# Performance work log

Measured on AMD Instinct MI355X. Metric: run time of the kernel, lower is better.

## Reference

```python
import jax, jax.numpy as jnp
import numpy as np

B, N, C = 4, 4096, 1024
H, HC = 16, 64
R = int(HC * np.log(HC))  # 266 random features
EPS = 1e-3


def _orthogonal_projection(num_rows, num_cols, seed=0):
    # Block-orthogonal random matrix: QR of gaussian blocks, rows concatenated.
    rng = np.random.default_rng(seed)
    blocks = []
    n_full = num_rows // num_cols
    for _ in range(n_full):
        q, _ = np.linalg.qr(rng.standard_normal((num_cols, num_cols)))
        blocks.append(q.T)
    remain = num_rows - n_full * num_cols
    if remain > 0:
        q, _ = np.linalg.qr(rng.standard_normal((num_cols, num_cols)))
        blocks.append(q.T[:remain])
    return np.concatenate(blocks, axis=0).astype(np.float32)  # (num_rows, num_cols)


def setup_inputs() -> dict:
    key = jax.random.key(0)
    ks = jax.random.split(key, 6)
    scale = 0.02
    return {
        "x": jax.random.normal(ks[0], (B, N, C), dtype=jnp.float32),
        "Wq": jax.random.normal(ks[1], (C, H * HC), dtype=jnp.float32) * scale,
        "Wk": jax.random.normal(ks[2], (C, H * HC), dtype=jnp.float32) * scale,
        "Wv": jax.random.normal(ks[3], (C, H * HC), dtype=jnp.float32) * scale,
        "Wo": jax.random.normal(ks[4], (H * HC, C), dtype=jnp.float32) * scale,
        "bo": jnp.zeros((C,), dtype=jnp.float32),
        "proj": jnp.asarray(_orthogonal_projection(R, HC, seed=0)),
    }


def reference(x, Wq, Wk, Wv, Wo, bo, proj):
    b, n, _ = x.shape
    # qkv projections, split heads: (B, H, N, HC)
    q = (x @ Wq).reshape(b, n, H, HC).transpose(0, 2, 1, 3)
    k = (x @ Wk).reshape(b, n, H, HC).transpose(0, 2, 1, 3)
    v = (x @ Wv).reshape(b, n, H, HC).transpose(0, 2, 1, 3)
    # FAVOR+ generalized kernel: relu(x @ proj^T) + eps -> (B, H, N, R)
    qp = jax.nn.relu(jnp.einsum('bhnd,rd->bhnr', q, proj)) + EPS
    kp = jax.nn.relu(jnp.einsum('bhnd,rd->bhnr', k, proj)) + EPS
    # linear attention: O(N) in sequence length
    k_sum = kp.sum(axis=-2)                                   # (B, H, R)
    d_inv = 1.0 / jnp.einsum('bhnr,bhr->bhn', qp, k_sum)      # (B, H, N)
    kv = jnp.einsum('bhnr,bhnd->bhrd', kp, v)                 # (B, H, R, HC)
    qkv = jnp.einsum('bhnr,bhrd->bhnd', qp, kv)               # (B, H, N, HC)
    out = qkv * d_inv[..., None]
    # merge heads and output projection
    out = out.transpose(0, 2, 1, 3).reshape(b, n, H * HC)
    return out @ Wo + bo
```

## Files before the change

kernel.cpp:

```cpp
#include <hip/hip_runtime.h>
#include <hip/hip_bf16.h>


typedef __bf16 bf16x8 __attribute__((ext_vector_type(8)));
typedef unsigned short u16x8 __attribute__((ext_vector_type(8)));
typedef float  f32x4  __attribute__((ext_vector_type(4)));

#define EPS_F 1e-3f

__device__ __forceinline__ void gld16(const void* g, void* l) {
  __builtin_amdgcn_global_load_lds(
      (const __attribute__((address_space(1))) void*)g,
      (__attribute__((address_space(3))) void*)l, 16, 0, 0);
}

template <int EPI>
__global__ void __launch_bounds__(512, 2)
gemm256(const __hip_bfloat16* __restrict__ A, long lda,
        const __hip_bfloat16* __restrict__ Bt, long ldb,
        void* __restrict__ Cp, long ldc,
        int Mtiles, int Ntiles, int K, const float* __restrict__ bias) {
  __shared__ __align__(16) char sm[131072];

  const int tid  = threadIdx.x;
  const int lane = tid & 63;
  const int wave = tid >> 6;
  const int wm   = wave >> 2;
  const int wn   = wave & 3;
  const int quad = lane >> 4;
  const int l15  = lane & 15;

  const int bid = blockIdx.x;
  const int Mx  = Mtiles >> 3;
  const int xcd = bid & 7;
  const int wl  = bid >> 3;
  const int gsz = Mx << 2;
  const int grp = wl / gsz;
  const int rr  = wl - grp * gsz;
  const int mt  = xcd * Mx + (rr % Mx);
  const int nt  = (grp << 2) + (rr / Mx);
  const long m0 = (long)mt * 256;
  const long n0 = (long)nt * 256;

  const int srow = tid >> 3;
  const int sg   = (tid & 7) ^ (srow & 7);
  const __hip_bfloat16* aS = A  + (m0 + srow) * lda + sg * 8;
  const __hip_bfloat16* bS = Bt + (n0 + srow) * ldb + sg * 8;
  char* smc = (char*)sm;
  const int ldsOff = tid * 16;

  const int aRowB = (wm * 128 + l15) * 128;
  const int bRowB = 32768 + (wn * 64 + l15) * 128;
  const int sw    = (l15 & 7) << 4;
  const int cx0   = (quad * 16) ^ sw;
  const int cx1   = (64 + quad * 16) ^ sw;

  f32x4 acc[8][4] = {};

#define GLD_A(pp, kk, i)                                                   \
  gld16(aS + (long)(i) * 64 * lda + (kk),                                  \
        smc + (pp) * 65536 + (i) * 8192 + ldsOff);
#define GLD_B(pp, kk, i)                                                   \
  gld16(bS + (long)(i) * 64 * ldb + (kk),                                  \
        smc + (pp) * 65536 + 32768 + (i) * 8192 + ldsOff);

#define QCL(AR, BR, accI, accJ)                                            \
  __builtin_amdgcn_s_setprio(1);                                           \
  _Pragma("unroll") for (int it = 0; it < 4; ++it)                         \
      _Pragma("unroll") for (int jt = 0; jt < 2; ++jt)                     \
          acc[(accI) + it][(accJ) + jt] =                                  \
              __builtin_amdgcn_mfma_f32_16x16x32_bf16(                     \
                  AR[it], BR[jt], acc[(accI) + it][(accJ) + jt], 0, 0, 0); \
  __builtin_amdgcn_s_setprio(0);

  const int NT = K >> 6;
#pragma unroll
  for (int i = 0; i < 4; ++i) { GLD_A(0, 0, i) GLD_B(0, 0, i) }
#pragma unroll
  for (int i = 0; i < 4; ++i) { GLD_A(1, 64, i) GLD_B(1, 64, i) }
  asm volatile("s_waitcnt vmcnt(8)" ::: "memory");
  __builtin_amdgcn_s_barrier();
  asm volatile("" ::: "memory");

  bf16x8 a0k0[4], a1k0[4], a0k1[4], a1k1[4];
  bf16x8 b01k0[2], b23k0[2], b01k1[2], b23k1[2];
#pragma unroll
  for (int jt = 0; jt < 2; ++jt)
    b01k0[jt] = *(const bf16x8*)(smc + bRowB + jt * 2048 + cx0);
#pragma unroll
  for (int it = 0; it < 4; ++it)
    a0k0[it] = *(const bf16x8*)(smc + aRowB + it * 2048 + cx0);

  int p = 0;
  for (int t = 0; t < NT; ++t) {
    const char* base  = smc + p * 65536;
    const char* nbase = smc + (p ^ 1) * 65536;
    const long kk = (long)(t + 2) * 64;
    const bool pf = (t + 2 < NT);

#pragma unroll
    for (int jt = 0; jt < 2; ++jt)
      b23k0[jt] = *(const bf16x8*)(base + bRowB + (jt + 2) * 2048 + cx0);
    QCL(a0k0, b01k0, 0, 0)
#pragma unroll
    for (int it = 0; it < 4; ++it)
      a1k0[it] = *(const bf16x8*)(base + aRowB + (4 + it) * 2048 + cx0);
    QCL(a0k0, b23k0, 0, 2)
#pragma unroll
    for (int jt = 0; jt < 2; ++jt)
      b01k1[jt] = *(const bf16x8*)(base + bRowB + jt * 2048 + cx1);
#pragma unroll
    for (int it = 0; it < 4; ++it)
      a0k1[it] = *(const bf16x8*)(base + aRowB + it * 2048 + cx1);
    QCL(a1k0, b01k0, 4, 0)
#pragma unroll
    for (int jt = 0; jt < 2; ++jt)
      b23k1[jt] = *(const bf16x8*)(base + bRowB + (jt + 2) * 2048 + cx1);
    QCL(a1k0, b23k0, 4, 2)
#pragma unroll
    for (int it = 0; it < 4; ++it)
      a1k1[it] = *(const bf16x8*)(base + aRowB + (4 + it) * 2048 + cx1);
    QCL(a0k1, b01k1, 0, 0)
    QCL(a0k1, b23k1, 0, 2)
    asm volatile("s_waitcnt lgkmcnt(0)" ::: "memory");
    __builtin_amdgcn_s_barrier();
    asm volatile("" ::: "memory");
    if (pf) {
      GLD_A(p, kk, 0) GLD_A(p, kk, 1) GLD_A(p, kk, 2) GLD_A(p, kk, 3)
      GLD_B(p, kk, 0) GLD_B(p, kk, 1) GLD_B(p, kk, 2) GLD_B(p, kk, 3)
    }
    QCL(a1k1, b01k1, 4, 0)
    if (pf) {
      asm volatile("s_waitcnt vmcnt(8)" ::: "memory");
    } else {
      asm volatile("s_waitcnt vmcnt(0)" ::: "memory");
    }
    __builtin_amdgcn_s_barrier();
    asm volatile("" ::: "memory");
    if (t + 1 < NT) {
#pragma unroll
      for (int jt = 0; jt < 2; ++jt)
        b01k0[jt] = *(const bf16x8*)(nbase + bRowB + jt * 2048 + cx0);
#pragma unroll
      for (int it = 0; it < 4; ++it)
        a0k0[it] = *(const bf16x8*)(nbase + aRowB + it * 2048 + cx0);
    }
    QCL(a1k1, b23k1, 4, 2)
    p ^= 1;
  }
#undef GLD_A
#undef GLD_B
#undef QCL

  if constexpr (EPI == 7) {
    __hip_bfloat16* Cb = (__hip_bfloat16*)Cp;
    const long slab  = (n0 >> 10) * 16777216;
    const long ncol0 = (n0 & 1023) + wn * 64 + l15;
#pragma unroll
    for (int it = 0; it < 8; ++it) {
#pragma unroll
      for (int i = 0; i < 4; ++i) {
        const long gm = m0 + wm * 128 + it * 16 + quad * 4 + i;
        __hip_bfloat16* rowp = Cb + slab + gm * 1024 + ncol0;
#pragma unroll
        for (int jt = 0; jt < 4; ++jt)
          rowp[jt * 16] = (__hip_bfloat16)acc[it][jt][i];
      }
    }
  } else if constexpr (EPI == 5) {
    float* Cf = (float*)Cp;
    float bv[4];
#pragma unroll
    for (int jt = 0; jt < 4; ++jt)
      bv[jt] = bias[n0 + wn * 64 + jt * 16 + l15];
#pragma unroll
    for (int it = 0; it < 8; ++it) {
#pragma unroll
      for (int i = 0; i < 4; ++i) {
        const long gm = m0 + wm * 128 + it * 16 + quad * 4 + i;
        float* rowp = Cf + gm * ldc + n0 + wn * 64 + l15;
#pragma unroll
        for (int jt = 0; jt < 4; ++jt)
          rowp[jt * 16] = acc[it][jt][i] + bv[jt];
      }
    }
  }
}

__global__ void __launch_bounds__(512, 2)
favor_kv(const __hip_bfloat16* __restrict__ Kb,
         const __hip_bfloat16* __restrict__ Vb,
         const __hip_bfloat16* __restrict__ projb_g,
         float* __restrict__ kvp) {
  __shared__ __align__(16) char sm[147456];
  char* Pj  = sm;
  char* KtB = sm + 36864;
  char* KPB = sm + 53248;
  char* VTB = sm + 126976;

  const int tid  = threadIdx.x;
  const int lane = tid & 63;
  const int wave = tid >> 6;
  const int quad = lane >> 4;
  const int l15  = lane & 15;
  const int swL  = (l15 & 7) << 4;

  const int bh   = blockIdx.x & 63;
  const int slab = blockIdx.x >> 6;
  const int b    = bh >> 4, h = bh & 15;
  const long rowbase = (long)b * 4096 + (long)slab * 1024;

  for (int p = 0; p < 5; ++p) {
    const int idx = p * 512 + tid;
    if (idx < 2304) {
      const int r = idx >> 3, g = (idx & 7) ^ (r & 7);
      gld16(projb_g + r * 64 + g * 8, Pj + idx * 16);
    }
  }
#pragma unroll
  for (int q = 0; q < 2; ++q) {
    unsigned short* vth = (unsigned short*)(VTB + q * 10240 + 64 * 128);
    for (int i = tid; i < 1024; i += 512) vth[i] = (i < 64) ? 0x3F80 : 0;
  }

  const int rK = tid >> 3, gK = (tid & 7) ^ (rK & 7);
  const int nl = tid >> 3, seg = tid & 7;
  gld16(Kb + (rowbase + rK) * 1024 + h * 64 + gK * 8, KtB + tid * 16);
  u16x8 vc = *(const u16x8*)(Vb + (rowbase + nl) * 1024 + h * 64 + seg * 8);

  const int wm1 = wave & 3;
  const int wn1 = wave >> 2;
  const int nJ  = (wave < 2) ? 3 : 2;

  f32x4 acc2[3][5] = {};

#define KV_GEMM2(KPo, VTo)                                                   \
  _Pragma("unroll") for (int ks = 0; ks < 2; ++ks) {                         \
    const int cb = ks * 64 + quad * 16;                                      \
    bf16x8 bfr2[5];                                                          \
    _Pragma("unroll") for (int fd = 0; fd < 5; ++fd) {                       \
      const int d = fd * 16 + l15;                                           \
      const int s2 = ((d & 7) ^ ((d >> 3) & 7)) << 4;                        \
      bfr2[fd] = *(const bf16x8*)((VTo) + d * 128 + (cb ^ s2));              \
    }                                                                        \
    _Pragma("unroll") for (int j = 0; j < 3; ++j) {                          \
      if (j < nJ) {                                                          \
        const int r2 = (wave + 8 * j) * 16 + l15;                            \
        const bf16x8 af2 =                                                   \
            *(const bf16x8*)((KPo) + r2 * 128 + (cb ^ ((r2 & 7) << 4)));     \
        _Pragma("unroll") for (int fd = 0; fd < 5; ++fd)                     \
            acc2[j][fd] = __builtin_amdgcn_mfma_f32_16x16x32_bf16(           \
                af2, bfr2[fd], acc2[j][fd], 0, 0, 0);                        \
      }                                                                      \
    }                                                                        \
  }

  for (int t = 0; t < 16; ++t) {
    const int q = t & 1;
    char* Kt  = KtB + q * 8192;
    char* KP  = KPB + q * 36864;
    char* VT  = VTB + q * 10240;
    char* KPo = KPB + (q ^ 1) * 36864;
    char* VTo = VTB + (q ^ 1) * 10240;

    asm volatile("s_waitcnt vmcnt(0)" ::: "memory");
    __builtin_amdgcn_s_barrier();
    asm volatile("" ::: "memory");

#pragma unroll
    for (int j = 0; j < 8; ++j) {
      const int d = seg * 8 + j;
      const int s = ((d & 7) ^ ((d >> 3) & 7)) << 4;
      *(unsigned short*)(VT + d * 128 + ((nl * 2) ^ s)) = vc[j];
    }
    if (t < 15) {
      const long nb1 = rowbase + (long)(t + 1) * 64;
      gld16(Kb + (nb1 + rK) * 1024 + h * 64 + gK * 8,
            KtB + (q ^ 1) * 8192 + tid * 16);
      vc = *(const u16x8*)(Vb + (nb1 + nl) * 1024 + h * 64 + seg * 8);
    }
    f32x4 acc1[9] = {};
#pragma unroll
    for (int ks = 0; ks < 2; ++ks) {
      const int cb = ks * 64 + quad * 16;
      const bf16x8 af1 =
          *(const bf16x8*)(Kt + (wm1 * 16 + l15) * 128 + (cb ^ swL));
      bf16x8 bfr[9];
#pragma unroll
      for (int fn = 0; fn < 9; ++fn)
        bfr[fn] = *(const bf16x8*)(Pj + (wn1 * 144 + fn * 16 + l15) * 128 +
                                   (cb ^ swL));
#pragma unroll
      for (int fn = 0; fn < 9; ++fn)
        acc1[fn] = __builtin_amdgcn_mfma_f32_16x16x32_bf16(af1, bfr[fn],
                                                           acc1[fn], 0, 0, 0);
    }
    {
      const int nb = (wm1 * 16 + quad * 4) * 2;
#pragma unroll
      for (int fn = 0; fn < 9; ++fn) {
        const int r = wn1 * 144 + fn * 16 + l15;
        const bool ok = (r < 266);
        union { __hip_bfloat16 hh[4]; uint2 u; } pk;
#pragma unroll
        for (int ii = 0; ii < 4; ++ii) {
          float v = acc1[fn][ii];
          v = ok ? (fmaxf(v, 0.f) + EPS_F) : 0.f;
          pk.hh[ii] = (__hip_bfloat16)v;
        }
        *(uint2*)(KP + r * 128 + (nb ^ ((r & 7) << 4))) = pk.u;
      }
    }
    if (t > 0) { KV_GEMM2(KPo, VTo) }
    asm volatile("s_waitcnt lgkmcnt(0)" ::: "memory");
    __builtin_amdgcn_s_barrier();
    asm volatile("" ::: "memory");
  }
  { KV_GEMM2(KPB + 36864, VTB + 10240) }
#undef KV_GEMM2

  float* dst = kvp + (long)blockIdx.x * 23040;
#pragma unroll
  for (int j = 0; j < 3; ++j) {
    if (j < nJ) {
      const int rb = (wave + 8 * j) * 16 + quad * 4;
#pragma unroll
      for (int fd = 0; fd < 5; ++fd) {
        const int d = fd * 16 + l15;
#pragma unroll
        for (int ii = 0; ii < 4; ++ii)
          dst[(long)(rb + ii) * 80 + d] = acc2[j][fd][ii];
      }
    }
  }
}

__global__ void __launch_bounds__(256)
finalize_kvx2(const float* __restrict__ kvp,
              __hip_bfloat16* __restrict__ kvxb) {
  __shared__ float lf[288 * 21];
  const int bh = blockIdx.x >> 2, dq = blockIdx.x & 3, t = threadIdx.x;
  for (int p = 0; p < 23; ++p) {
    const int q = p * 256 + t;
    if (q < 5760) {
      const int r = q / 20, dl = q - r * 20;
      float s = 0.f;
#pragma unroll
      for (int sl = 0; sl < 4; ++sl)
        s += kvp[(long)(sl * 64 + bh) * 23040 + r * 80 + dq * 20 + dl];
      lf[r * 21 + dl] = s;
    }
  }
  __syncthreads();
  for (int p = 0; p < 23; ++p) {
    const int o = p * 256 + t;
    if (o < 5760) {
      const int dl = o / 288, r = o - dl * 288;
      kvxb[(long)bh * 23040 + (long)(dq * 20 + dl) * 288 + r] =
          (__hip_bfloat16)lf[r * 21 + dl];
    }
  }
}

__global__ void __launch_bounds__(512, 2)
favor_out(const __hip_bfloat16* __restrict__ Qb,
          const __hip_bfloat16* __restrict__ kvxb_g,
          const __hip_bfloat16* __restrict__ projb_g,
          __hip_bfloat16* __restrict__ outm) {
  __shared__ __align__(16) char sm[160512];
  char* Pj = sm;
  char* KX = sm + 36864;
  char* QP = sm + 84224;
  float* Dsh = (float*)(sm + 160000);

  const int tid  = threadIdx.x;
  const int lane = tid & 63;
  const int wave = tid >> 6;
  const int quad = lane >> 4;
  const int l15  = lane & 15;
  const int swL  = (l15 & 7) << 4;

  const int bh  = blockIdx.x >> 3;
  const int rb8 = blockIdx.x & 7;
  const int b = bh >> 4, h = bh & 15;
  const long rowbase = (long)b * 4096 + (long)rb8 * 512;

  for (int p = 0; p < 5; ++p) {
    const int idx = p * 512 + tid;
    if (idx < 2304) {
      const int r = idx >> 3, g = (idx & 7) ^ (r & 7);
      gld16(projb_g + r * 64 + g * 8, Pj + idx * 16);
    }
  }
  {
    const __hip_bfloat16* src = kvxb_g + (long)bh * 23040;
#pragma unroll
    for (int p = 0; p < 6; ++p) {
      const int idx = p * 512 + tid;
      if (idx < 2880) {
        const int d = idx / 36, g = idx % 36;
        const bf16x8 v = *(const bf16x8*)(src + d * 288 + g * 8);
        *(bf16x8*)(KX + d * 592 + g * 16) = v;
      }
    }
  }
  const int rS = tid >> 3, gS = (tid & 7) ^ (rS & 7);
  const int rS2 = rS + 64, gS2 = (tid & 7) ^ (rS2 & 7);
  u16x8 qv0 = *(const u16x8*)(Qb + (rowbase + rS) * 1024 + h * 64 + gS * 8);
  u16x8 qv1 = *(const u16x8*)(Qb + (rowbase + rS2) * 1024 + h * 64 + gS2 * 8);

  const int wm1 = wave >> 2;
  const int wn1 = wave & 3;

  for (int s = 0; s < 4; ++s) {
    *(u16x8*)(QP + tid * 16) = qv0;
    *(u16x8*)(QP + 8192 + tid * 16) = qv1;
    asm volatile("s_waitcnt lgkmcnt(0)" ::: "memory");
    if (s == 0) asm volatile("s_waitcnt vmcnt(0)" ::: "memory");
    __builtin_amdgcn_s_barrier();
    asm volatile("" ::: "memory");
    f32x4 acc1[9][2] = {};
#pragma unroll
    for (int ks = 0; ks < 2; ++ks) {
      const int cb = ks * 64 + quad * 16;
      bf16x8 bfr[2];
#pragma unroll
      for (int fn = 0; fn < 2; ++fn)
        bfr[fn] = *(const bf16x8*)(QP + (wn1 * 32 + fn * 16 + l15) * 128 +
                                   (cb ^ swL));
      bf16x8 af[9];
#pragma unroll
      for (int fm = 0; fm < 9; ++fm)
        af[fm] = *(const bf16x8*)(Pj + (wm1 * 144 + fm * 16 + l15) * 128 +
                                  (cb ^ swL));
#pragma unroll
      for (int fm = 0; fm < 9; ++fm)
#pragma unroll
        for (int fn = 0; fn < 2; ++fn)
          acc1[fm][fn] = __builtin_amdgcn_mfma_f32_16x16x32_bf16(
              af[fm], bfr[fn], acc1[fm][fn], 0, 0, 0);
    }
    if (s < 3) {
      const long n1 = (long)(s + 1) * 128;
      qv0 = *(const u16x8*)(Qb + (rowbase + n1 + rS) * 1024 + h * 64 + gS * 8);
      qv1 = *(const u16x8*)(Qb + (rowbase + n1 + rS2) * 1024 + h * 64 +
                            gS2 * 8);
    }
    __builtin_amdgcn_s_barrier();
    asm volatile("" ::: "memory");
#pragma unroll
    for (int fm = 0; fm < 9; ++fm) {
      const int r0 = wm1 * 144 + fm * 16 + quad * 4;
#pragma unroll
      for (int fn = 0; fn < 2; ++fn) {
        const int n = wn1 * 32 + fn * 16 + l15;
        union { __hip_bfloat16 hh[4]; uint2 u; } pk;
#pragma unroll
        for (int ii = 0; ii < 4; ++ii) {
          float v = acc1[fm][fn][ii];
          v = (r0 + ii < 266) ? (fmaxf(v, 0.f) + EPS_F) : 0.f;
          pk.hh[ii] = (__hip_bfloat16)v;
        }
        *(uint2*)(QP + n * 592 + r0 * 2) = pk.u;
      }
    }
    asm volatile("s_waitcnt lgkmcnt(0)" ::: "memory");
    __builtin_amdgcn_s_barrier();
    asm volatile("" ::: "memory");
    f32x4 acc2[5] = {};
#pragma unroll
    for (int ks = 0; ks < 9; ++ks) {
      const int cb = ks * 64 + quad * 16;
      const bf16x8 af = *(const bf16x8*)(QP + (wave * 16 + l15) * 592 + cb);
      bf16x8 bfr[5];
#pragma unroll
      for (int fd = 0; fd < 5; ++fd)
        bfr[fd] = *(const bf16x8*)(KX + (fd * 16 + l15) * 592 + cb);
#pragma unroll
      for (int fd = 0; fd < 5; ++fd)
        acc2[fd] = __builtin_amdgcn_mfma_f32_16x16x32_bf16(af, bfr[fd],
                                                           acc2[fd], 0, 0, 0);
    }
    if (l15 == 0) {
#pragma unroll
      for (int ii = 0; ii < 4; ++ii)
        Dsh[wave * 16 + quad * 4 + ii] = acc2[4][ii];
    }
    asm volatile("s_waitcnt lgkmcnt(0)" ::: "memory");
    __builtin_amdgcn_s_barrier();
    asm volatile("" ::: "memory");
#pragma unroll
    for (int ii = 0; ii < 4; ++ii) {
      const int nloc = wave * 16 + quad * 4 + ii;
      const float den = Dsh[nloc];
      const float dinv = (den > 1e-30f) ? (1.f / den) : 0.f;
      __hip_bfloat16* rowp =
          outm + (rowbase + (long)s * 128 + nloc) * 1024 + h * 64;
#pragma unroll
      for (int fd = 0; fd < 4; ++fd)
        rowp[fd * 16 + l15] = (__hip_bfloat16)(acc2[fd][ii] * dinv);
    }
  }
}

__global__ void cvt_x(const float* __restrict__ x,
                      __hip_bfloat16* __restrict__ xb) {
  const long i = ((long)blockIdx.x * 256 + threadIdx.x) * 8;
  const float4 f0 = *(const float4*)(x + i);
  const float4 f1 = *(const float4*)(x + i + 4);
  union { __hip_bfloat16 h[8]; uint4 u; } r;
  r.h[0] = (__hip_bfloat16)f0.x; r.h[1] = (__hip_bfloat16)f0.y;
  r.h[2] = (__hip_bfloat16)f0.z; r.h[3] = (__hip_bfloat16)f0.w;
  r.h[4] = (__hip_bfloat16)f1.x; r.h[5] = (__hip_bfloat16)f1.y;
  r.h[6] = (__hip_bfloat16)f1.z; r.h[7] = (__hip_bfloat16)f1.w;
  *(uint4*)(xb + i) = r.u;
}

__global__ void prep_w(const float* __restrict__ s0,
                       const float* __restrict__ s1,
                       const float* __restrict__ s2,
                       const float* __restrict__ s3,
                       const float* __restrict__ proj,
                       __hip_bfloat16* __restrict__ dq,
                       __hip_bfloat16* __restrict__ dwo,
                       __hip_bfloat16* __restrict__ projb) {
  const int z = blockIdx.z;
  if (z == 4) {
    const int i = (blockIdx.y * 32 + blockIdx.x) * 256 + (int)threadIdx.x;
    if (i < 288 * 64) {
      const int r = i >> 6;
      __hip_bfloat16 v = (__hip_bfloat16)0.f;
      if (r < 266) v = (__hip_bfloat16)proj[i];
      projb[i] = v;
    }
    return;
  }
  __shared__ float t[32][33];
  const float* src = (z == 0) ? s0 : (z == 1) ? s1 : (z == 2) ? s2 : s3;
  __hip_bfloat16* dst = (z < 3) ? (dq + (long)z * 1048576) : dwo;
  const int k0 = blockIdx.x * 32, n0 = blockIdx.y * 32;
  const int tx = threadIdx.x & 31, ty = threadIdx.x >> 5;
#pragma unroll
  for (int i = 0; i < 4; ++i)
    t[ty + i * 8][tx] = src[(long)(k0 + ty + i * 8) * 1024 + n0 + tx];
  __syncthreads();
#pragma unroll
  for (int i = 0; i < 4; ++i)
    dst[(long)(n0 + ty + i * 8) * 1024 + k0 + tx] =
        (__hip_bfloat16)t[tx][ty + i * 8];
}

extern "C" void kernel_launch(void* const* d_in, const int* in_sizes, int n_in,
                              void* d_out, int out_size, void* d_ws,
                              size_t ws_size, hipStream_t stream) {
  const float* x    = (const float*)d_in[0];
  const float* Wq   = (const float*)d_in[1];
  const float* Wk   = (const float*)d_in[2];
  const float* Wv   = (const float*)d_in[3];
  const float* Wo   = (const float*)d_in[4];
  const float* bo   = (const float*)d_in[5];
  const float* proj = (const float*)d_in[6];
  float* out = (float*)d_out;
  char* ws = (char*)d_ws;

  constexpr long o_wqkvt = 0;
  constexpr long o_wot   = 6291456;
  constexpr long o_projb = 8388608;
  constexpr long o_Qb    = 8425472;
  constexpr long o_Kb    = 41979904;
  constexpr long o_Vb    = 75534336;
  constexpr long o_xb    = 109088768;
  constexpr long o_kvp   = 109088768;
  constexpr long o_kvxb  = 132681728;

  __hip_bfloat16* wqkvt = (__hip_bfloat16*)(ws + o_wqkvt);
  __hip_bfloat16* wot   = (__hip_bfloat16*)(ws + o_wot);
  __hip_bfloat16* projb = (__hip_bfloat16*)(ws + o_projb);
  __hip_bfloat16* Qb    = (__hip_bfloat16*)(ws + o_Qb);
  __hip_bfloat16* Kb    = (__hip_bfloat16*)(ws + o_Kb);
  __hip_bfloat16* Vb    = (__hip_bfloat16*)(ws + o_Vb);
  __hip_bfloat16* xb    = (__hip_bfloat16*)(ws + o_xb);
  float*          kvp   = (float*)(ws + o_kvp);
  __hip_bfloat16* kvxb  = (__hip_bfloat16*)(ws + o_kvxb);
  __hip_bfloat16* outm  = Kb;

  cvt_x<<<8192, 256, 0, stream>>>(x, xb);
  prep_w<<<dim3(32, 32, 5), 256, 0, stream>>>(Wq, Wk, Wv, Wo, proj, wqkvt,
                                              wot, projb);

  gemm256<7><<<768, 512, 0, stream>>>(xb, 1024, wqkvt, 1024, Qb, 0, 64, 12,
                                      1024, nullptr);

  favor_kv<<<256, 512, 0, stream>>>(Kb, Vb, projb, kvp);
  finalize_kvx2<<<256, 256, 0, stream>>>(kvp, kvxb);

  favor_out<<<512, 512, 0, stream>>>(Qb, kvxb, projb, outm);

  gemm256<5><<<256, 512, 0, stream>>>(outm, 1024, wot, 1024, out, 1024, 64, 4,
                                      1024, bo);
}
```

Baseline: 367.3 us.

## Double-buffer Q tiles via async LDS loads and read kv straight from global

```diff
diff --git a/kernel.cpp b/kernel.cpp
--- a/kernel.cpp
+++ b/kernel.cpp
@@ -367,11 +367,10 @@
           const __hip_bfloat16* __restrict__ kvxb_g,
           const __hip_bfloat16* __restrict__ projb_g,
           __hip_bfloat16* __restrict__ outm) {
-  __shared__ __align__(16) char sm[160512];
-  char* Pj = sm;
-  char* KX = sm + 36864;
-  char* QP = sm + 84224;
-  float* Dsh = (float*)(sm + 160000);
+  __shared__ __align__(16) char sm[145408];
+  char* Pj  = sm;
+  char* QbL = sm + 36864;
+  char* QP  = sm + 69632;
 
   const int tid  = threadIdx.x;
   const int lane = tid & 63;
@@ -384,6 +383,7 @@
   const int rb8 = blockIdx.x & 7;
   const int b = bh >> 4, h = bh & 15;
   const long rowbase = (long)b * 4096 + (long)rb8 * 512;
+  const __hip_bfloat16* kx = kvxb_g + (long)bh * 23040;
 
   for (int p = 0; p < 5; ++p) {
     const int idx = p * 512 + tid;
@@ -392,31 +392,18 @@
       gld16(projb_g + r * 64 + g * 8, Pj + idx * 16);
     }
   }
-  {
-    const __hip_bfloat16* src = kvxb_g + (long)bh * 23040;
-#pragma unroll
-    for (int p = 0; p < 6; ++p) {
-      const int idx = p * 512 + tid;
-      if (idx < 2880) {
-        const int d = idx / 36, g = idx % 36;
-        const bf16x8 v = *(const bf16x8*)(src + d * 288 + g * 8);
-        *(bf16x8*)(KX + d * 592 + g * 16) = v;
-      }
-    }
-  }
   const int rS = tid >> 3, gS = (tid & 7) ^ (rS & 7);
   const int rS2 = rS + 64, gS2 = (tid & 7) ^ (rS2 & 7);
-  u16x8 qv0 = *(const u16x8*)(Qb + (rowbase + rS) * 1024 + h * 64 + gS * 8);
-  u16x8 qv1 = *(const u16x8*)(Qb + (rowbase + rS2) * 1024 + h * 64 + gS2 * 8);
+  gld16(Qb + (rowbase + rS) * 1024 + h * 64 + gS * 8, QbL + tid * 16);
+  gld16(Qb + (rowbase + rS2) * 1024 + h * 64 + gS2 * 8, QbL + 8192 + tid * 16);
 
   const int wm1 = wave >> 2;
   const int wn1 = wave & 3;
 
   for (int s = 0; s < 4; ++s) {
-    *(u16x8*)(QP + tid * 16) = qv0;
-    *(u16x8*)(QP + 8192 + tid * 16) = qv1;
-    asm volatile("s_waitcnt lgkmcnt(0)" ::: "memory");
-    if (s == 0) asm volatile("s_waitcnt vmcnt(0)" ::: "memory");
+    const int q = s & 1;
+    const char* Qcur = QbL + q * 16384;
+    asm volatile("s_waitcnt vmcnt(0)" ::: "memory");
     __builtin_amdgcn_s_barrier();
     asm volatile("" ::: "memory");
     f32x4 acc1[9][2] = {};
@@ -426,7 +413,7 @@
       bf16x8 bfr[2];
 #pragma unroll
       for (int fn = 0; fn < 2; ++fn)
-        bfr[fn] = *(const bf16x8*)(QP + (wn1 * 32 + fn * 16 + l15) * 128 +
+        bfr[fn] = *(const bf16x8*)(Qcur + (wn1 * 32 + fn * 16 + l15) * 128 +
                                    (cb ^ swL));
       bf16x8 af[9];
 #pragma unroll
@@ -441,13 +428,12 @@
               af[fm], bfr[fn], acc1[fm][fn], 0, 0, 0);
     }
     if (s < 3) {
-      const long n1 = (long)(s + 1) * 128;
-      qv0 = *(const u16x8*)(Qb + (rowbase + n1 + rS) * 1024 + h * 64 + gS * 8);
-      qv1 = *(const u16x8*)(Qb + (rowbase + n1 + rS2) * 1024 + h * 64 +
-                            gS2 * 8);
-    }
-    __builtin_amdgcn_s_barrier();
-    asm volatile("" ::: "memory");
+      const long n1 = rowbase + (long)(s + 1) * 128;
+      gld16(Qb + (n1 + rS) * 1024 + h * 64 + gS * 8,
+            QbL + (q ^ 1) * 16384 + tid * 16);
+      gld16(Qb + (n1 + rS2) * 1024 + h * 64 + gS2 * 8,
+            QbL + (q ^ 1) * 16384 + 8192 + tid * 16);
+    }
 #pragma unroll
     for (int fm = 0; fm < 9; ++fm) {
       const int r0 = wm1 * 144 + fm * 16 + quad * 4;
@@ -475,25 +461,18 @@
       bf16x8 bfr[5];
 #pragma unroll
       for (int fd = 0; fd < 5; ++fd)
-        bfr[fd] = *(const bf16x8*)(KX + (fd * 16 + l15) * 592 + cb);
+        bfr[fd] = *(const bf16x8*)(kx + (fd * 16 + l15) * 288 + ks * 32 +
+                                   quad * 8);
 #pragma unroll
       for (int fd = 0; fd < 5; ++fd)
         acc2[fd] = __builtin_amdgcn_mfma_f32_16x16x32_bf16(af, bfr[fd],
                                                            acc2[fd], 0, 0, 0);
     }
-    if (l15 == 0) {
-#pragma unroll
-      for (int ii = 0; ii < 4; ++ii)
-        Dsh[wave * 16 + quad * 4 + ii] = acc2[4][ii];
-    }
-    asm volatile("s_waitcnt lgkmcnt(0)" ::: "memory");
-    __builtin_amdgcn_s_barrier();
-    asm volatile("" ::: "memory");
 #pragma unroll
     for (int ii = 0; ii < 4; ++ii) {
+      const float den = __shfl(acc2[4][ii], quad << 4, 64);
+      const float dinv = (den > 1e-30f) ? (1.f / den) : 0.f;
       const int nloc = wave * 16 + quad * 4 + ii;
-      const float den = Dsh[nloc];
-      const float dinv = (den > 1e-30f) ? (1.f / den) : 0.f;
       __hip_bfloat16* rowp =
           outm + (rowbase + (long)s * 128 + nloc) * 1024 + h * 64;
 #pragma unroll
```

Measured after the change: 395.4 us. 1.08x slower.

## Load Q fragments directly from global and broadcast denominators via shuffles

Applied to the files above, without the earlier changes.

```diff
diff --git a/kernel.cpp b/kernel.cpp
--- a/kernel.cpp
+++ b/kernel.cpp
@@ -362,16 +362,15 @@
   }
 }
 
-__global__ void __launch_bounds__(512, 2)
+__global__ void __launch_bounds__(512, 1)
 favor_out(const __hip_bfloat16* __restrict__ Qb,
           const __hip_bfloat16* __restrict__ kvxb_g,
           const __hip_bfloat16* __restrict__ projb_g,
           __hip_bfloat16* __restrict__ outm) {
-  __shared__ __align__(16) char sm[160512];
+  __shared__ __align__(16) char sm[160000];
   char* Pj = sm;
   char* KX = sm + 36864;
   char* QP = sm + 84224;
-  float* Dsh = (float*)(sm + 160000);
 
   const int tid  = threadIdx.x;
   const int lane = tid & 63;
@@ -404,21 +403,13 @@
       }
     }
   }
-  const int rS = tid >> 3, gS = (tid & 7) ^ (rS & 7);
-  const int rS2 = rS + 64, gS2 = (tid & 7) ^ (rS2 & 7);
-  u16x8 qv0 = *(const u16x8*)(Qb + (rowbase + rS) * 1024 + h * 64 + gS * 8);
-  u16x8 qv1 = *(const u16x8*)(Qb + (rowbase + rS2) * 1024 + h * 64 + gS2 * 8);
+  __syncthreads();
 
   const int wm1 = wave >> 2;
   const int wn1 = wave & 3;
 
   for (int s = 0; s < 4; ++s) {
-    *(u16x8*)(QP + tid * 16) = qv0;
-    *(u16x8*)(QP + 8192 + tid * 16) = qv1;
-    asm volatile("s_waitcnt lgkmcnt(0)" ::: "memory");
-    if (s == 0) asm volatile("s_waitcnt vmcnt(0)" ::: "memory");
-    __builtin_amdgcn_s_barrier();
-    asm volatile("" ::: "memory");
+    const long qrow = rowbase + (long)s * 128;
     f32x4 acc1[9][2] = {};
 #pragma unroll
     for (int ks = 0; ks < 2; ++ks) {
@@ -426,8 +417,9 @@
       bf16x8 bfr[2];
 #pragma unroll
       for (int fn = 0; fn < 2; ++fn)
-        bfr[fn] = *(const bf16x8*)(QP + (wn1 * 32 + fn * 16 + l15) * 128 +
-                                   (cb ^ swL));
+        bfr[fn] = *(const bf16x8*)(Qb +
+                                   (qrow + wn1 * 32 + fn * 16 + l15) * 1024 +
+                                   h * 64 + ks * 32 + quad * 8);
       bf16x8 af[9];
 #pragma unroll
       for (int fm = 0; fm < 9; ++fm)
@@ -440,14 +432,6 @@
           acc1[fm][fn] = __builtin_amdgcn_mfma_f32_16x16x32_bf16(
               af[fm], bfr[fn], acc1[fm][fn], 0, 0, 0);
     }
-    if (s < 3) {
-      const long n1 = (long)(s + 1) * 128;
-      qv0 = *(const u16x8*)(Qb + (rowbase + n1 + rS) * 1024 + h * 64 + gS * 8);
-      qv1 = *(const u16x8*)(Qb + (rowbase + n1 + rS2) * 1024 + h * 64 +
-                            gS2 * 8);
-    }
-    __builtin_amdgcn_s_barrier();
-    asm volatile("" ::: "memory");
 #pragma unroll
     for (int fm = 0; fm < 9; ++fm) {
       const int r0 = wm1 * 144 + fm * 16 + quad * 4;
@@ -481,25 +465,18 @@
         acc2[fd] = __builtin_amdgcn_mfma_f32_16x16x32_bf16(af, bfr[fd],
                                                            acc2[fd], 0, 0, 0);
     }
-    if (l15 == 0) {
-#pragma unroll
-      for (int ii = 0; ii < 4; ++ii)
-        Dsh[wave * 16 + quad * 4 + ii] = acc2[4][ii];
-    }
-    asm volatile("s_waitcnt lgkmcnt(0)" ::: "memory");
+#pragma unroll
+    for (int ii = 0; ii < 4; ++ii) {
+      const float den = __shfl(acc2[4][ii], quad << 4, 64);
+      const float dinv = (den > 1e-30f) ? (1.f / den) : 0.f;
+      const int nloc = wave * 16 + quad * 4 + ii;
+      __hip_bfloat16* rowp = outm + (qrow + nloc) * 1024 + h * 64;
+#pragma unroll
+      for (int fd = 0; fd < 4; ++fd)
+        rowp[fd * 16 + l15] = (__hip_bfloat16)(acc2[fd][ii] * dinv);
+    }
     __builtin_amdgcn_s_barrier();
     asm volatile("" ::: "memory");
-#pragma unroll
-    for (int ii = 0; ii < 4; ++ii) {
-      const int nloc = wave * 16 + quad * 4 + ii;
-      const float den = Dsh[nloc];
-      const float dinv = (den > 1e-30f) ? (1.f / den) : 0.f;
-      __hip_bfloat16* rowp =
-          outm + (rowbase + (long)s * 128 + nloc) * 1024 + h * 64;
-#pragma unroll
-      for (int fd = 0; fd < 4; ++fd)
-        rowp[fd * 16 + l15] = (__hip_bfloat16)(acc2[fd][ii] * dinv);
-    }
   }
 }
 
```

Result: no change. 370.9 us (+1.0%).
